# Optimization experiments

Measured on AMD Instinct MI355X. Metric: run time of the kernel, lower is better.

The kernel has to match this reference:

```python
import jax, jax.numpy as jnp
import numpy as np

N, E, D, H, C, G = 50000, 800000, 128, 128, 16, 512


def setup_inputs() -> dict:
    key = jax.random.key(0)
    ks = jax.random.split(key, 8)

    def glorot(k, shape):
        lim = float(np.sqrt(6.0 / (shape[0] + shape[1])))
        return jax.random.uniform(k, shape, jnp.float32, -lim, lim)

    x = jax.random.normal(ks[0], (N, D), jnp.float32)
    edge_index = jax.random.randint(ks[1], (2, E), 0, N, dtype=jnp.int32)
    batch = jnp.sort(jax.random.randint(ks[2], (N,), 0, G, dtype=jnp.int32))
    return {
        'x': x,
        'edge_index': edge_index,
        'batch': batch,
        'W1': glorot(ks[3], (D, H)), 'b1': jnp.zeros((H,), jnp.float32),
        'W2': glorot(ks[4], (H, H)), 'b2': jnp.zeros((H,), jnp.float32),
        'lW1': glorot(ks[5], (4 * H, 2 * H)), 'lb1': jnp.zeros((2 * H,), jnp.float32),
        'lW2': glorot(ks[6], (2 * H, C)), 'lb2': jnp.zeros((C,), jnp.float32),
    }


def _gcn_norm(edge_index, n):
    # add self loops, then symmetric normalization D^-1/2 (A+I) D^-1/2
    loop = jnp.arange(n, dtype=edge_index.dtype)
    src = jnp.concatenate([edge_index[0], loop])
    dst = jnp.concatenate([edge_index[1], loop])
    ones = jnp.ones(src.shape[0], jnp.float32)
    deg = jax.ops.segment_sum(ones, dst, num_segments=n)
    dis = jnp.where(deg > 0, jax.lax.rsqrt(jnp.maximum(deg, 1.0)), 0.0)
    norm = dis[src] * dis[dst]  # [E+N]
    return src, dst, norm


def _gcn_conv(x, src, dst, norm, W, b, n):
    h = x @ W                                   # [N, H] transform first (PyG order)
    msg = h[src] * norm[:, None]                # gather + normalize, [E+N, H]
    out = jax.ops.segment_sum(msg, dst, num_segments=n)  # scatter-add
    return out + b


def _pool(x, batch, g):
    cnt = jax.ops.segment_sum(jnp.ones(x.shape[0], x.dtype), batch, num_segments=g)
    mean = jax.ops.segment_sum(x, batch, num_segments=g) / jnp.maximum(cnt, 1.0)[:, None]
    mx = jax.ops.segment_max(x, batch, num_segments=g)
    mx = jnp.where(cnt[:, None] > 0, mx, 0.0)
    return mean, mx


def reference(x, edge_index, batch, W1, b1, W2, b2, lW1, lb1, lW2, lb2):
    n = x.shape[0]
    src, dst, norm = _gcn_norm(edge_index, n)
    x0 = jax.nn.relu(_gcn_conv(x, src, dst, norm, W1, b1, n))   # dropout=identity (eval)
    g0_mean, g0_max = _pool(x0, batch, G)
    x1 = jax.nn.relu(_gcn_conv(x0, src, dst, norm, W2, b2, n))
    g1_mean, g1_max = _pool(x1, batch, G)
    g = jnp.concatenate([g0_mean, g0_max, g1_mean, g1_max], axis=-1)  # [G, 4H]
    h = jax.nn.relu(g @ lW1 + lb1)
    return h @ lW2 + lb2  # [G, C]
```

## Files before the change

kernel.cpp:

```cpp
#include <hip/hip_runtime.h>
#include <hip/hip_bf16.h>

#define NN 50000
#define EE 800000
#define DD 128
#define HH 128
#define CC 16
#define GG 512
#define NBLK_SCAN 196
#define NPAD 50176
#define GEMM_BLOCKS 782
#define POOLF (4 * GG * HH + GG)
#define EQ 200000

typedef __attribute__((ext_vector_type(8))) short short8v;
typedef __attribute__((ext_vector_type(8))) unsigned short ushort8v;
typedef __attribute__((ext_vector_type(4))) float f32x4;

__device__ inline unsigned short f2bf(float x) {
    unsigned int u = __float_as_uint(x);
    u += 0x7fffu + ((u >> 16) & 1u);
    return (unsigned short)(u >> 16);
}

__global__ __launch_bounds__(256) void k_init(const float* __restrict__ W1, const float* __restrict__ W2,
                                              unsigned short* __restrict__ Wf,
                                              int* __restrict__ deg, float* __restrict__ pools) {
    int tid = blockIdx.x * 256 + threadIdx.x;
    int nt = gridDim.x * 256;
    for (int i = tid; i < NPAD; i += nt) deg[i] = 0;
    for (int i = tid; i < POOLF; i += nt) pools[i] = 0.0f;
    for (int idx = tid; idx < 4096; idx += nt) {
        const float* W = (idx >> 11) ? W2 : W1;
        int id2 = idx & 2047;
        int lane = id2 & 63, ct = (id2 >> 6) & 7, kt = id2 >> 9;
        int col = ct * 16 + (lane & 15);
        int k0 = kt * 32 + (lane >> 4) * 8;
        ushort8v v;
        #pragma unroll
        for (int j = 0; j < 8; ++j) v[j] = f2bf(W[(k0 + j) * 128 + col]);
        *(ushort8v*)(Wf + idx * 8) = v;
    }
}

__global__ __launch_bounds__(256) void k_deg(const int* __restrict__ ei, int* __restrict__ deg) {
    int e = blockIdx.x * 256 + threadIdx.x;
    if (e < EE) atomicAdd(&deg[ei[EE + e]], 1);
}

__global__ __launch_bounds__(256) void k_scan1(const int* __restrict__ deg,
                                               int* __restrict__ offs, int* __restrict__ bsum,
                                               float* __restrict__ dis) {
    __shared__ int tmp[256];
    int i = blockIdx.x * 256 + threadIdx.x;
    int v = (i < NN) ? deg[i] : 0;
    if (i < NN) dis[i] = rsqrtf((float)v + 1.0f);
    tmp[threadIdx.x] = v;
    __syncthreads();
    for (int off = 1; off < 256; off <<= 1) {
        int t = (threadIdx.x >= off) ? tmp[threadIdx.x - off] : 0;
        __syncthreads();
        tmp[threadIdx.x] += t;
        __syncthreads();
    }
    if (i < NN) offs[i] = tmp[threadIdx.x] - v;
    if (threadIdx.x == 255) bsum[blockIdx.x] = tmp[255];
}

__global__ __launch_bounds__(256) void k_scan2(int* __restrict__ bsum) {
    __shared__ int tmp[256];
    int v = (threadIdx.x < NBLK_SCAN) ? bsum[threadIdx.x] : 0;
    tmp[threadIdx.x] = v;
    __syncthreads();
    for (int off = 1; off < 256; off <<= 1) {
        int t = (threadIdx.x >= off) ? tmp[threadIdx.x - off] : 0;
        __syncthreads();
        tmp[threadIdx.x] += t;
        __syncthreads();
    }
    bsum[threadIdx.x] = tmp[threadIdx.x] - v;
}

__global__ __launch_bounds__(256) void k_scan3(int* __restrict__ offs, const int* __restrict__ bsum,
                                               int* __restrict__ cursor) {
    int i = blockIdx.x * 256 + threadIdx.x;
    if (i < NN) {
        int v = offs[i] + bsum[blockIdx.x];
        offs[i] = v;
        cursor[i] = v;
    }
}

__global__ __launch_bounds__(256) void k_fill(const int* __restrict__ ei, const float* __restrict__ dis,
                                              int* __restrict__ cursor, unsigned int* __restrict__ adj) {
    int base = blockIdx.x * 256 + threadIdx.x;
    if (base >= EQ) return;
    int s0 = ei[base];            int d0 = ei[EE + base];
    int s1 = ei[base + EQ];       int d1 = ei[EE + base + EQ];
    int s2 = ei[base + 2 * EQ];   int d2 = ei[EE + base + 2 * EQ];
    int s3 = ei[base + 3 * EQ];   int d3 = ei[EE + base + 3 * EQ];
    float n0 = dis[s0] * dis[d0];
    float n1 = dis[s1] * dis[d1];
    float n2 = dis[s2] * dis[d2];
    float n3 = dis[s3] * dis[d3];
    int p0 = atomicAdd(&cursor[d0], 1);
    int p1 = atomicAdd(&cursor[d1], 1);
    int p2 = atomicAdd(&cursor[d2], 1);
    int p3 = atomicAdd(&cursor[d3], 1);
    adj[p0] = ((unsigned int)s0 << 16) | (unsigned int)f2bf(n0);
    adj[p1] = ((unsigned int)s1 << 16) | (unsigned int)f2bf(n1);
    adj[p2] = ((unsigned int)s2 << 16) | (unsigned int)f2bf(n2);
    adj[p3] = ((unsigned int)s3 << 16) | (unsigned int)f2bf(n3);
}

__global__ __launch_bounds__(256) void k_gemm(const float* __restrict__ Af,
                                              const unsigned short* __restrict__ Ab,
                                              const unsigned short* __restrict__ Wf,
                                              unsigned short* __restrict__ O,
                                              int af32) {
    __shared__ unsigned short Wl[16384];
    #pragma unroll
    for (int idx = threadIdx.x; idx < 2048; idx += 256)
        *(ushort8v*)(Wl + idx * 8) = *(const ushort8v*)(Wf + idx * 8);
    __syncthreads();

    int wid = threadIdx.x >> 6, lane = threadIdx.x & 63;
    int b = lane >> 4;
    int row = blockIdx.x * 64 + wid * 16 + (lane & 15);

    short8v a[4];
    if (af32) {
        int r = min(row, NN - 1);
        const float* ap = Af + (size_t)r * 128 + b * 8;
        #pragma unroll
        for (int kt = 0; kt < 4; ++kt) {
            float4 f0 = *(const float4*)(ap + kt * 32);
            float4 f1 = *(const float4*)(ap + kt * 32 + 4);
            short8v v;
            v[0] = (short)f2bf(f0.x); v[1] = (short)f2bf(f0.y);
            v[2] = (short)f2bf(f0.z); v[3] = (short)f2bf(f0.w);
            v[4] = (short)f2bf(f1.x); v[5] = (short)f2bf(f1.y);
            v[6] = (short)f2bf(f1.z); v[7] = (short)f2bf(f1.w);
            a[kt] = v;
        }
    } else {
        const unsigned short* ap = Ab + (size_t)row * 128 + b * 8;
        #pragma unroll
        for (int kt = 0; kt < 4; ++kt) a[kt] = *(const short8v*)(ap + kt * 32);
    }

    f32x4 z = 0.0f;
    f32x4 acc[8] = {z, z, z, z, z, z, z, z};
    #pragma unroll
    for (int kt = 0; kt < 4; ++kt) {
        #pragma unroll
        for (int ct = 0; ct < 8; ++ct) {
            short8v bfrag = *(const short8v*)(Wl + ((kt * 8 + ct) * 64 + lane) * 8);
            acc[ct] = __builtin_amdgcn_mfma_f32_16x16x32_bf16(a[kt], bfrag, acc[ct], 0, 0, 0);
        }
    }

    int orow = blockIdx.x * 64 + wid * 16 + b * 4;
    unsigned short* op = O + (size_t)orow * 128 + (lane & 15);
    #pragma unroll
    for (int j = 0; j < 4; ++j) {
        #pragma unroll
        for (int ct = 0; ct < 8; ++ct)
            op[(size_t)j * 128 + ct * 16] = f2bf(acc[ct][j]);
    }
}

__global__ __launch_bounds__(256) void k_conv(const unsigned short* __restrict__ h,
                                              const unsigned int* __restrict__ adj,
                                              const int* __restrict__ row_start,
                                              const int* __restrict__ deg,
                                              const float* __restrict__ dis,
                                              const float* __restrict__ bias,
                                              const int* __restrict__ batch,
                                              unsigned short* __restrict__ xout,
                                              float* __restrict__ gsum,
                                              float* __restrict__ gmax,
                                              float* __restrict__ cnt,
                                              int flags) {
    __shared__ float lacc[16][128];
    __shared__ int lb[16];
    const int tid = threadIdx.x;
    const int wid = tid >> 6, lane = tid & 63;
    const int g = lane >> 4, l = lane & 15;
    const int nrow = wid * 4 + g;
    const int node = blockIdx.x * 16 + nrow;
    const int fb = l * 8;

    const float di = dis[node];
    const float d2 = di * di;
    const uint4 hv = *(const uint4*)(h + (size_t)node * 128 + fb);
    const float4 bv0 = *(const float4*)(bias + fb);
    const float4 bv1 = *(const float4*)(bias + fb + 4);
    float acc[8];
    acc[0] = __uint_as_float(hv.x << 16)         * d2 + bv0.x;
    acc[1] = __uint_as_float(hv.x & 0xffff0000u) * d2 + bv0.y;
    acc[2] = __uint_as_float(hv.y << 16)         * d2 + bv0.z;
    acc[3] = __uint_as_float(hv.y & 0xffff0000u) * d2 + bv0.w;
    acc[4] = __uint_as_float(hv.z << 16)         * d2 + bv1.x;
    acc[5] = __uint_as_float(hv.z & 0xffff0000u) * d2 + bv1.y;
    acc[6] = __uint_as_float(hv.w << 16)         * d2 + bv1.z;
    acc[7] = __uint_as_float(hv.w & 0xffff0000u) * d2 + bv1.w;

    const int rs = row_start[node];
    const int n  = deg[node];
    const unsigned int* ap = adj + rs;
    const int sl = lane & 48;
    const int nfull = n & ~15;

    for (int k = 0; k < nfull; k += 16) {
        unsigned int e = ap[k + l];
        #pragma unroll
        for (int j = 0; j < 16; ++j) {
            unsigned int ej = __shfl(e, sl + j);
            float w = __uint_as_float(ej << 16);
            const uint4 v = *(const uint4*)(h + (size_t)(ej >> 16) * 128 + fb);
            acc[0] = fmaf(__uint_as_float(v.x << 16),         w, acc[0]);
            acc[1] = fmaf(__uint_as_float(v.x & 0xffff0000u), w, acc[1]);
            acc[2] = fmaf(__uint_as_float(v.y << 16),         w, acc[2]);
            acc[3] = fmaf(__uint_as_float(v.y & 0xffff0000u), w, acc[3]);
            acc[4] = fmaf(__uint_as_float(v.z << 16),         w, acc[4]);
            acc[5] = fmaf(__uint_as_float(v.z & 0xffff0000u), w, acc[5]);
            acc[6] = fmaf(__uint_as_float(v.w << 16),         w, acc[6]);
            acc[7] = fmaf(__uint_as_float(v.w & 0xffff0000u), w, acc[7]);
        }
    }
    if (nfull < n) {
        unsigned int e = ap[min(nfull + l, n - 1)];
        #pragma unroll
        for (int j = 0; j < 16; ++j) {
            unsigned int ej = __shfl(e, sl + j);
            float w = (nfull + j < n) ? __uint_as_float(ej << 16) : 0.0f;
            const uint4 v = *(const uint4*)(h + (size_t)(ej >> 16) * 128 + fb);
            acc[0] = fmaf(__uint_as_float(v.x << 16),         w, acc[0]);
            acc[1] = fmaf(__uint_as_float(v.x & 0xffff0000u), w, acc[1]);
            acc[2] = fmaf(__uint_as_float(v.y << 16),         w, acc[2]);
            acc[3] = fmaf(__uint_as_float(v.y & 0xffff0000u), w, acc[3]);
            acc[4] = fmaf(__uint_as_float(v.z << 16),         w, acc[4]);
            acc[5] = fmaf(__uint_as_float(v.z & 0xffff0000u), w, acc[5]);
            acc[6] = fmaf(__uint_as_float(v.w << 16),         w, acc[6]);
            acc[7] = fmaf(__uint_as_float(v.w & 0xffff0000u), w, acc[7]);
        }
    }
    #pragma unroll
    for (int p = 0; p < 8; ++p) acc[p] = fmaxf(acc[p], 0.0f);

    if (flags & 1) {
        uint4 o;
        o.x = (unsigned)f2bf(acc[0]) | ((unsigned)f2bf(acc[1]) << 16);
        o.y = (unsigned)f2bf(acc[2]) | ((unsigned)f2bf(acc[3]) << 16);
        o.z = (unsigned)f2bf(acc[4]) | ((unsigned)f2bf(acc[5]) << 16);
        o.w = (unsigned)f2bf(acc[6]) | ((unsigned)f2bf(acc[7]) << 16);
        *(uint4*)(xout + (size_t)node * 128 + fb) = o;
    }

    #pragma unroll
    for (int p = 0; p < 8; ++p) lacc[nrow][fb + p] = acc[p];
    if (l == 0) lb[nrow] = batch[node];
    __syncthreads();
    {
        const int f = tid & 127;
        const bool domax = tid >= 128;
        float s = lacc[0][f];
        int cur = lb[0], run = 1;
        #pragma unroll
        for (int w = 1; w < 16; ++w) {
            float a = lacc[w][f];
            if (lb[w] == cur) {
                s = domax ? fmaxf(s, a) : (s + a);
                ++run;
            } else {
                if (domax) {
                    atomicMax((int*)&gmax[cur * 128 + f], __float_as_int(s));
                } else {
                    atomicAdd(&gsum[cur * 128 + f], s);
                    if (f == 0 && (flags & 2)) atomicAdd(cnt + cur, (float)run);
                }
                s = a; cur = lb[w]; run = 1;
            }
        }
        if (domax) {
            atomicMax((int*)&gmax[cur * 128 + f], __float_as_int(s));
        } else {
            atomicAdd(&gsum[cur * 128 + f], s);
            if (f == 0 && (flags & 2)) atomicAdd(cnt + cur, (float)run);
        }
    }
}

__global__ __launch_bounds__(256) void k_mlp(const float* __restrict__ gsum0,
                                             const float* __restrict__ gmax0,
                                             const float* __restrict__ gsum1,
                                             const float* __restrict__ gmax1,
                                             const float* __restrict__ cnt,
                                             const float* __restrict__ lW1,
                                             const float* __restrict__ lb1,
                                             const float* __restrict__ lW2,
                                             const float* __restrict__ lb2,
                                             float* __restrict__ out) {
    __shared__ float gl[512];
    __shared__ float hb[256];
    __shared__ float part[256];
    int r = blockIdx.x;
    float inv = 1.0f / fmaxf(cnt[r], 1.0f);
    for (int k = threadIdx.x; k < 512; k += 256) {
        int seg = k >> 7, f = k & 127;
        float v;
        if (seg == 0)      v = gsum0[r * 128 + f] * inv;
        else if (seg == 1) v = gmax0[r * 128 + f];
        else if (seg == 2) v = gsum1[r * 128 + f] * inv;
        else               v = gmax1[r * 128 + f];
        gl[k] = v;
    }
    __syncthreads();
    {
        int j = threadIdx.x;
        float acc = lb1[j];
        for (int k = 0; k < 512; ++k) acc += gl[k] * lW1[k * 256 + j];
        hb[j] = fmaxf(acc, 0.f);
    }
    __syncthreads();
    {
        int c = threadIdx.x & 15, ch = threadIdx.x >> 4;
        float p = 0.f;
        #pragma unroll
        for (int j2 = 0; j2 < 16; ++j2) p += hb[ch * 16 + j2] * lW2[(ch * 16 + j2) * 16 + c];
        part[threadIdx.x] = p;
    }
    __syncthreads();
    if (threadIdx.x < 16) {
        float s = lb2[threadIdx.x];
        #pragma unroll
        for (int ch2 = 0; ch2 < 16; ++ch2) s += part[ch2 * 16 + threadIdx.x];
        out[r * 16 + threadIdx.x] = s;
    }
}

extern "C" void kernel_launch(void* const* d_in, const int* in_sizes, int n_in,
                              void* d_out, int out_size, void* d_ws, size_t ws_size,
                              hipStream_t stream) {
    const float* x    = (const float*)d_in[0];
    const int*   ei   = (const int*)d_in[1];
    const int*   batch= (const int*)d_in[2];
    const float* W1   = (const float*)d_in[3];
    const float* b1   = (const float*)d_in[4];
    const float* W2   = (const float*)d_in[5];
    const float* b2   = (const float*)d_in[6];
    const float* lW1  = (const float*)d_in[7];
    const float* lb1  = (const float*)d_in[8];
    const float* lW2  = (const float*)d_in[9];
    const float* lb2  = (const float*)d_in[10];
    float* out = (float*)d_out;

    unsigned short* hbuf = (unsigned short*)d_ws;
    unsigned short* x0b  = hbuf + (size_t)NPAD * 128;
    unsigned short* wf   = x0b + (size_t)NPAD * 128;
    float* dis   = (float*)(wf + 32768);
    float* gsum0 = dis + NPAD;
    float* gmax0 = gsum0 + GG * HH;
    float* gsum1 = gmax0 + GG * HH;
    float* gmax1 = gsum1 + GG * HH;
    float* cnt   = gmax1 + GG * HH;
    int*   deg    = (int*)(cnt + GG);
    int*   offs   = deg + NPAD;
    int*   cursor = offs + NPAD;
    int*   bsum   = cursor + NPAD;
    unsigned int* adj = (unsigned int*)(bsum + 256);

    k_init<<<256, 256, 0, stream>>>(W1, W2, wf, deg, gsum0);

    k_deg<<<(EE + 255) / 256, 256, 0, stream>>>(ei, deg);
    k_scan1<<<NBLK_SCAN, 256, 0, stream>>>(deg, offs, bsum, dis);
    k_scan2<<<1, 256, 0, stream>>>(bsum);
    k_scan3<<<NBLK_SCAN, 256, 0, stream>>>(offs, bsum, cursor);
    k_fill<<<(EQ + 255) / 256, 256, 0, stream>>>(ei, dis, cursor, adj);

    k_gemm<<<GEMM_BLOCKS, 256, 0, stream>>>(x, (const unsigned short*)nullptr, wf, hbuf, 1);
    k_conv<<<NN / 16, 256, 0, stream>>>(hbuf, adj, offs, deg, dis, b1, batch,
                                        x0b, gsum0, gmax0, cnt, 3);
    k_gemm<<<GEMM_BLOCKS, 256, 0, stream>>>((const float*)nullptr, x0b, wf + 16384, hbuf, 0);
    k_conv<<<NN / 16, 256, 0, stream>>>(hbuf, adj, offs, deg, dis, b2, batch,
                                        x0b, gsum1, gmax1, cnt, 0);

    k_mlp<<<GG, 256, 0, stream>>>(gsum0, gmax0, gsum1, gmax1, cnt, lW1, lb1, lW2, lb2, out);
}
```

Measured before the change: 219.8 us.

## Merge scan passes and co-launch adjacency fill with first-layer GEMM

New measurement: 205.1 us. 1.07x faster.

```diff
diff --git a/kernel.cpp b/kernel.cpp
--- a/kernel.cpp
+++ b/kernel.cpp
@@ -10,8 +10,8 @@
 #define NBLK_SCAN 196
 #define NPAD 50176
 #define GEMM_BLOCKS 782
+#define FILL_BLOCKS 3125
 #define POOLF (4 * GG * HH + GG)
-#define EQ 200000
 
 typedef __attribute__((ext_vector_type(8))) short short8v;
 typedef __attribute__((ext_vector_type(8))) unsigned short ushort8v;
@@ -67,71 +67,45 @@
     if (threadIdx.x == 255) bsum[blockIdx.x] = tmp[255];
 }
 
-__global__ __launch_bounds__(256) void k_scan2(int* __restrict__ bsum) {
-    __shared__ int tmp[256];
-    int v = (threadIdx.x < NBLK_SCAN) ? bsum[threadIdx.x] : 0;
-    tmp[threadIdx.x] = v;
-    __syncthreads();
-    for (int off = 1; off < 256; off <<= 1) {
-        int t = (threadIdx.x >= off) ? tmp[threadIdx.x - off] : 0;
+__global__ __launch_bounds__(256) void k_scan23(int* __restrict__ offs, const int* __restrict__ bsum,
+                                                int* __restrict__ cursor) {
+    __shared__ int sdata[256];
+    int t = threadIdx.x;
+    sdata[t] = (t < (int)blockIdx.x && t < NBLK_SCAN) ? bsum[t] : 0;
+    __syncthreads();
+    for (int off = 128; off > 0; off >>= 1) {
+        if (t < off) sdata[t] += sdata[t + off];
         __syncthreads();
-        tmp[threadIdx.x] += t;
-        __syncthreads();
-    }
-    bsum[threadIdx.x] = tmp[threadIdx.x] - v;
-}
-
-__global__ __launch_bounds__(256) void k_scan3(int* __restrict__ offs, const int* __restrict__ bsum,
-                                               int* __restrict__ cursor) {
-    int i = blockIdx.x * 256 + threadIdx.x;
+    }
+    int base = sdata[0];
+    int i = blockIdx.x * 256 + t;
     if (i < NN) {
-        int v = offs[i] + bsum[blockIdx.x];
+        int v = offs[i] + base;
         offs[i] = v;
         cursor[i] = v;
     }
 }
 
-__global__ __launch_bounds__(256) void k_fill(const int* __restrict__ ei, const float* __restrict__ dis,
-                                              int* __restrict__ cursor, unsigned int* __restrict__ adj) {
-    int base = blockIdx.x * 256 + threadIdx.x;
-    if (base >= EQ) return;
-    int s0 = ei[base];            int d0 = ei[EE + base];
-    int s1 = ei[base + EQ];       int d1 = ei[EE + base + EQ];
-    int s2 = ei[base + 2 * EQ];   int d2 = ei[EE + base + 2 * EQ];
-    int s3 = ei[base + 3 * EQ];   int d3 = ei[EE + base + 3 * EQ];
-    float n0 = dis[s0] * dis[d0];
-    float n1 = dis[s1] * dis[d1];
-    float n2 = dis[s2] * dis[d2];
-    float n3 = dis[s3] * dis[d3];
-    int p0 = atomicAdd(&cursor[d0], 1);
-    int p1 = atomicAdd(&cursor[d1], 1);
-    int p2 = atomicAdd(&cursor[d2], 1);
-    int p3 = atomicAdd(&cursor[d3], 1);
-    adj[p0] = ((unsigned int)s0 << 16) | (unsigned int)f2bf(n0);
-    adj[p1] = ((unsigned int)s1 << 16) | (unsigned int)f2bf(n1);
-    adj[p2] = ((unsigned int)s2 << 16) | (unsigned int)f2bf(n2);
-    adj[p3] = ((unsigned int)s3 << 16) | (unsigned int)f2bf(n3);
-}
-
-__global__ __launch_bounds__(256) void k_gemm(const float* __restrict__ Af,
-                                              const unsigned short* __restrict__ Ab,
-                                              const unsigned short* __restrict__ Wf,
-                                              unsigned short* __restrict__ O,
-                                              int af32) {
+__global__ __launch_bounds__(256) void k_fillgemm(const float* __restrict__ Af,
+                                                  const unsigned short* __restrict__ Wf,
+                                                  unsigned short* __restrict__ O,
+                                                  const int* __restrict__ ei,
+                                                  const float* __restrict__ dis,
+                                                  int* __restrict__ cursor,
+                                                  unsigned int* __restrict__ adj) {
     __shared__ unsigned short Wl[16384];
-    #pragma unroll
-    for (int idx = threadIdx.x; idx < 2048; idx += 256)
-        *(ushort8v*)(Wl + idx * 8) = *(const ushort8v*)(Wf + idx * 8);
-    __syncthreads();
-
-    int wid = threadIdx.x >> 6, lane = threadIdx.x & 63;
-    int b = lane >> 4;
-    int row = blockIdx.x * 64 + wid * 16 + (lane & 15);
-
-    short8v a[4];
-    if (af32) {
+    if (blockIdx.x < GEMM_BLOCKS) {
+        #pragma unroll
+        for (int idx = threadIdx.x; idx < 2048; idx += 256)
+            *(ushort8v*)(Wl + idx * 8) = *(const ushort8v*)(Wf + idx * 8);
+        __syncthreads();
+
+        int wid = threadIdx.x >> 6, lane = threadIdx.x & 63;
+        int b = lane >> 4;
+        int row = blockIdx.x * 64 + wid * 16 + (lane & 15);
         int r = min(row, NN - 1);
         const float* ap = Af + (size_t)r * 128 + b * 8;
+        short8v a[4];
         #pragma unroll
         for (int kt = 0; kt < 4; ++kt) {
             float4 f0 = *(const float4*)(ap + kt * 32);
@@ -143,11 +117,52 @@
             v[6] = (short)f2bf(f1.z); v[7] = (short)f2bf(f1.w);
             a[kt] = v;
         }
+        f32x4 z = 0.0f;
+        f32x4 acc[8] = {z, z, z, z, z, z, z, z};
+        #pragma unroll
+        for (int kt = 0; kt < 4; ++kt) {
+            #pragma unroll
+            for (int ct = 0; ct < 8; ++ct) {
+                short8v bfrag = *(const short8v*)(Wl + ((kt * 8 + ct) * 64 + lane) * 8);
+                acc[ct] = __builtin_amdgcn_mfma_f32_16x16x32_bf16(a[kt], bfrag, acc[ct], 0, 0, 0);
+            }
+        }
+        int orow = blockIdx.x * 64 + wid * 16 + b * 4;
+        unsigned short* op = O + (size_t)orow * 128 + (lane & 15);
+        #pragma unroll
+        for (int j = 0; j < 4; ++j) {
+            #pragma unroll
+            for (int ct = 0; ct < 8; ++ct)
+                op[(size_t)j * 128 + ct * 16] = f2bf(acc[ct][j]);
+        }
     } else {
-        const unsigned short* ap = Ab + (size_t)row * 128 + b * 8;
-        #pragma unroll
-        for (int kt = 0; kt < 4; ++kt) a[kt] = *(const short8v*)(ap + kt * 32);
-    }
+        int e = (blockIdx.x - GEMM_BLOCKS) * 256 + threadIdx.x;
+        if (e < EE) {
+            int s = ei[e];
+            int d = ei[EE + e];
+            float nrm = dis[s] * dis[d];
+            int pos = atomicAdd(&cursor[d], 1);
+            adj[pos] = ((unsigned int)s << 16) | (unsigned int)f2bf(nrm);
+        }
+    }
+}
+
+__global__ __launch_bounds__(256) void k_gemm(const unsigned short* __restrict__ Ab,
+                                              const unsigned short* __restrict__ Wf,
+                                              unsigned short* __restrict__ O) {
+    __shared__ unsigned short Wl[16384];
+    #pragma unroll
+    for (int idx = threadIdx.x; idx < 2048; idx += 256)
+        *(ushort8v*)(Wl + idx * 8) = *(const ushort8v*)(Wf + idx * 8);
+    __syncthreads();
+
+    int wid = threadIdx.x >> 6, lane = threadIdx.x & 63;
+    int b = lane >> 4;
+    int row = blockIdx.x * 64 + wid * 16 + (lane & 15);
+    const unsigned short* ap = Ab + (size_t)row * 128 + b * 8;
+    short8v a[4];
+    #pragma unroll
+    for (int kt = 0; kt < 4; ++kt) a[kt] = *(const short8v*)(ap + kt * 32);
 
     f32x4 z = 0.0f;
     f32x4 acc[8] = {z, z, z, z, z, z, z, z};
@@ -159,7 +174,6 @@
             acc[ct] = __builtin_amdgcn_mfma_f32_16x16x32_bf16(a[kt], bfrag, acc[ct], 0, 0, 0);
         }
     }
-
     int orow = blockIdx.x * 64 + wid * 16 + b * 4;
     unsigned short* op = O + (size_t)orow * 128 + (lane & 15);
     #pragma unroll
@@ -375,14 +389,13 @@
 
     k_deg<<<(EE + 255) / 256, 256, 0, stream>>>(ei, deg);
     k_scan1<<<NBLK_SCAN, 256, 0, stream>>>(deg, offs, bsum, dis);
-    k_scan2<<<1, 256, 0, stream>>>(bsum);
-    k_scan3<<<NBLK_SCAN, 256, 0, stream>>>(offs, bsum, cursor);
-    k_fill<<<(EQ + 255) / 256, 256, 0, stream>>>(ei, dis, cursor, adj);
-
-    k_gemm<<<GEMM_BLOCKS, 256, 0, stream>>>(x, (const unsigned short*)nullptr, wf, hbuf, 1);
+    k_scan23<<<NBLK_SCAN, 256, 0, stream>>>(offs, bsum, cursor);
+
+    k_fillgemm<<<GEMM_BLOCKS + FILL_BLOCKS, 256, 0, stream>>>(x, wf, hbuf, ei, dis, cursor, adj);
+
     k_conv<<<NN / 16, 256, 0, stream>>>(hbuf, adj, offs, deg, dis, b1, batch,
                                         x0b, gsum0, gmax0, cnt, 3);
-    k_gemm<<<GEMM_BLOCKS, 256, 0, stream>>>((const float*)nullptr, x0b, wf + 16384, hbuf, 0);
+    k_gemm<<<GEMM_BLOCKS, 256, 0, stream>>>(x0b, wf + 16384, hbuf);
     k_conv<<<NN / 16, 256, 0, stream>>>(hbuf, adj, offs, deg, dis, b2, batch,
                                         x0b, gsum1, gmax1, cnt, 0);
 
```
